# Optimization experiments

Hardware: AMD Instinct MI355X
Metric: run time of the kernel (lower is better)

## Reference

```python
import jax, jax.numpy as jnp
import numpy as np
from jax import lax

H = 64   # hidden_size
IN = 18  # input_size
L = 4    # lstm_layers
OUT = 3  # output_size
B = 2048
T = 512


def _lstm_layer(x, W_ih, W_hh, b_ih, b_hh):
    # x: [B,T,D]; PyTorch gate order: i, f, g, o
    xg = jnp.einsum('btd,gd->btg', x, W_ih) + b_ih + b_hh  # [B,T,4H]

    def step(carry, xg_t):
        h, c = carry
        gates = xg_t + h @ W_hh.T
        i, f, g, o = jnp.split(gates, 4, axis=-1)
        c = jax.nn.sigmoid(f) * c + jax.nn.sigmoid(i) * jnp.tanh(g)
        h = jax.nn.sigmoid(o) * jnp.tanh(c)
        return (h, c), h

    h0 = jnp.zeros((x.shape[0], H), x.dtype)
    _, hs = lax.scan(step, (h0, h0), jnp.swapaxes(xg, 0, 1))  # hs: [T,B,H]
    return jnp.swapaxes(hs, 0, 1)  # [B,T,H]


def _forward(x, Wi0, Wh0, bi0, bh0, Wi1, Wh1, bi1, bh1,
             Wi2, Wh2, bi2, bh2, Wi3, Wh3, bi3, bh3, W1, b1, W2, b2):
    h = x
    layers = [(Wi0, Wh0, bi0, bh0), (Wi1, Wh1, bi1, bh1),
              (Wi2, Wh2, bi2, bh2), (Wi3, Wh3, bi3, bh3)]
    for Wi, Wh, bi, bh in layers:
        h = _lstm_layer(h, Wi, Wh, bi, bh)
    last = h[:, -1, :]                      # [B,H]
    hid = jax.nn.relu(last @ W1.T + b1)     # [B,128]
    return hid @ W2.T + b2                  # [B,OUT]


def setup_inputs():
    key = jax.random.key(0)
    ks = jax.random.split(key, 1 + 4 * L + 4)
    d = {'x': jax.random.normal(ks[0], (B, T, IN), jnp.float32)}
    k = 1
    s = 0.1
    for l in range(L):
        din = IN if l == 0 else H
        d[f'Wi{l}'] = jax.random.normal(ks[k], (4 * H, din), jnp.float32) * s; k += 1
        d[f'Wh{l}'] = jax.random.normal(ks[k], (4 * H, H), jnp.float32) * s; k += 1
        d[f'bi{l}'] = jax.random.normal(ks[k], (4 * H,), jnp.float32) * s; k += 1
        d[f'bh{l}'] = jax.random.normal(ks[k], (4 * H,), jnp.float32) * s; k += 1
    d['W1'] = jax.random.normal(ks[k], (128, H), jnp.float32) * s; k += 1
    d['b1'] = jax.random.normal(ks[k], (128,), jnp.float32) * s; k += 1
    d['W2'] = jax.random.normal(ks[k], (OUT, 128), jnp.float32) * s; k += 1
    d['b2'] = jax.random.normal(ks[k], (OUT,), jnp.float32) * s
    return d


def reference(x, Wi0, Wh0, bi0, bh0, Wi1, Wh1, bi1, bh1,
              Wi2, Wh2, bi2, bh2, Wi3, Wh3, bi3, bh3, W1, b1, W2, b2):
    return _forward(x, Wi0, Wh0, bi0, bh0, Wi1, Wh1, bi1, bh1,
                    Wi2, Wh2, bi2, bh2, Wi3, Wh3, bi3, bh3, W1, b1, W2, b2)
```

## Files before the change

### kernel.cpp

```cpp
#include <hip/hip_runtime.h>
#include <stdint.h>

typedef __bf16 bf16_t;
typedef __bf16 bf16x8 __attribute__((ext_vector_type(8)));
typedef float  f32x4  __attribute__((ext_vector_type(4)));

union Frag { uint32_t u[4]; bf16x8 v; };

struct WPtrs {
    const float* Wi[4];
    const float* Wh[4];
    const float* bi[4];
    const float* bh[4];
};

#define LOG2E 1.44269504088896340736f

__device__ __forceinline__ float cell_c(float gi, float gf, float gg, float c) {
    const float ef = __builtin_amdgcn_exp2f(-gf);
    const float ei = __builtin_amdgcn_exp2f(-gi);
    const float Eg = __builtin_amdgcn_exp2f(gg);
    const float pf = 1.0f + ef, pi = 1.0f + ei;
    const float pg = Eg + 1.0f, mg = Eg - 1.0f;
    const float num = c * pi * pg + mg * pf;
    const float den = pf * pi * pg;
    return num * __builtin_amdgcn_rcpf(den);
}
__device__ __forceinline__ float cell_h(float go, float c) {
    const float Ec = __builtin_amdgcn_exp2f(c * (2.0f * LOG2E));
    const float eo = __builtin_amdgcn_exp2f(-go);
    const float num = Ec - 1.0f;
    const float den = (1.0f + eo) * (Ec + 1.0f);
    return num * __builtin_amdgcn_rcpf(den);
}

__device__ __forceinline__ float dpp_halfswap(float x) {
    int i = __float_as_int(x);
    int r = __builtin_amdgcn_update_dpp(i, i, 0x128 , 0xF, 0xF, false);
    return __int_as_float(r);
}

__global__ __launch_bounds__(1024, 4)
void lstm_fused(const float* __restrict__ x0, float* __restrict__ last_out, WPtrs wp)
{
    const int tile = blockIdx.x;
    const int tid  = threadIdx.x;
    const int w    = tid >> 6;
    const int lane = tid & 63;
    const int l15  = lane & 15;
    const int l4   = lane >> 4;
    const int l    = w >> 2;
    const int uq   = w & 3;
    const bool hiH = (l15 >= 8);
    const int  col = l15 & 7;

    __shared__ uint2 lds_h[2][4][64][6];

    for (int i = tid; i < 2 * 4 * 64 * 6; i += 1024)
        ((uint2*)lds_h)[i] = make_uint2(0u, 0u);

    const float* Wi = wp.Wi[l];
    const float* Wh = wp.Wh[l];

    const float gs[4] = {LOG2E, LOG2E, 2.0f * LOG2E, LOG2E};

    bf16x8 whA[4][2];
    bf16x8 wiA[4][2];
#pragma unroll
    for (int G = 0; G < 4; ++G) {
        const float sc = gs[G];
        const int row = G * 64 + 16 * uq + l15;
        const float* r = Wh + (size_t)row * 64;
#pragma unroll
        for (int s = 0; s < 2; ++s) {
            f32x4 a = *(const f32x4*)(r + 32 * s + 4 * l4);
            f32x4 b = *(const f32x4*)(r + 32 * s + 4 * l4 + 16);
            bf16x8 f;
            f[0] = (bf16_t)(a[0] * sc); f[1] = (bf16_t)(a[1] * sc);
            f[2] = (bf16_t)(a[2] * sc); f[3] = (bf16_t)(a[3] * sc);
            f[4] = (bf16_t)(b[0] * sc); f[5] = (bf16_t)(b[1] * sc);
            f[6] = (bf16_t)(b[2] * sc); f[7] = (bf16_t)(b[3] * sc);
            whA[G][s] = f;
        }
        if (l == 0) {
            const float* ri = Wi + (size_t)row * 18;
            const int k0 = 4 * l4;
            bf16x8 f;
            f[0] = (bf16_t)(ri[k0 + 0] * sc); f[1] = (bf16_t)(ri[k0 + 1] * sc);
            f[2] = (bf16_t)(ri[k0 + 2] * sc); f[3] = (bf16_t)(ri[k0 + 3] * sc);
            f[4] = (l4 == 0) ? (bf16_t)(ri[16] * sc) : (bf16_t)0.0f;
            f[5] = (l4 == 0) ? (bf16_t)(ri[17] * sc) : (bf16_t)0.0f;
            f[6] = (bf16_t)0.0f; f[7] = (bf16_t)0.0f;
            wiA[G][0] = f;
            wiA[G][1] = f;
        } else {
            const float* ri = Wi + (size_t)row * 64;
#pragma unroll
            for (int s = 0; s < 2; ++s) {
                f32x4 a = *(const f32x4*)(ri + 32 * s + 4 * l4);
                f32x4 b = *(const f32x4*)(ri + 32 * s + 4 * l4 + 16);
                bf16x8 f;
                f[0] = (bf16_t)(a[0] * sc); f[1] = (bf16_t)(a[1] * sc);
                f[2] = (bf16_t)(a[2] * sc); f[3] = (bf16_t)(a[3] * sc);
                f[4] = (bf16_t)(b[0] * sc); f[5] = (bf16_t)(b[1] * sc);
                f[6] = (bf16_t)(b[2] * sc); f[7] = (bf16_t)(b[3] * sc);
                wiA[G][s] = f;
            }
        }
    }

    float biasA[4], biasB[4];
#pragma unroll
    for (int G = 0; G < 4; ++G) {
        const int rb = G * 64 + 16 * uq + 4 * l4 + (hiH ? 2 : 0);
        biasA[G] = (wp.bi[l][rb]     + wp.bh[l][rb])     * gs[G];
        biasB[G] = (wp.bi[l][rb + 1] + wp.bh[l][rb + 1]) * gs[G];
    }

    bf16x8& xfA = wiA[2][1];
    bf16x8& xfB = wiA[3][1];
    const int    xbatch = tile * 8 + (hiH ? 7 : col);
    const float* xrow   = x0 + (size_t)xbatch * (512 * 18);
    auto loadx = [&](int t, bf16x8& dst) {
        const float* xr = xrow + t * 18;
        const int k0 = 4 * l4;
        bf16x8 f;
        f[0] = (bf16_t)xr[k0 + 0]; f[1] = (bf16_t)xr[k0 + 1];
        f[2] = (bf16_t)xr[k0 + 2]; f[3] = (bf16_t)xr[k0 + 3];
        f[4] = (l4 == 0) ? (bf16_t)xr[16] : (bf16_t)0.0f;
        f[5] = (l4 == 0) ? (bf16_t)xr[17] : (bf16_t)0.0f;
        f[6] = (bf16_t)0.0f; f[7] = (bf16_t)0.0f;
        dst = f;
    };
    if (l == 0) { loadx(0, xfA); loadx(1, xfB); }

    float c0 = 0.0f, c1 = 0.0f;

    __syncthreads();

    auto phase = [&](int p, int br, int bw, bf16x8& xf) {
        const int t = p - l;
        if (t >= 0 && t < 512) {
            const f32x4 z4 = {0.0f, 0.0f, 0.0f, 0.0f};
            f32x4 acc[4];

            if (l == 0) {
#pragma unroll
                for (int G = 0; G < 4; ++G)
                    acc[G] = __builtin_amdgcn_mfma_f32_16x16x32_bf16(wiA[G][0], xf, z4, 0, 0, 0);
                loadx((t + 2) & 511, xf);
            } else {
                Frag b0, b1;
                {
                    uint4 q0 = *(const uint4*)&lds_h[br][l - 1][lane][0];
                    uint4 q1 = *(const uint4*)&lds_h[br][l - 1][lane][2];
                    b0.u[0] = q0.x; b0.u[1] = q0.y; b0.u[2] = q0.z; b0.u[3] = q0.w;
                    b1.u[0] = q1.x; b1.u[1] = q1.y; b1.u[2] = q1.z; b1.u[3] = q1.w;
                }
#pragma unroll
                for (int G = 0; G < 4; ++G)
                    acc[G] = __builtin_amdgcn_mfma_f32_16x16x32_bf16(wiA[G][0], b0.v, z4, 0, 0, 0);
#pragma unroll
                for (int G = 0; G < 4; ++G)
                    acc[G] = __builtin_amdgcn_mfma_f32_16x16x32_bf16(wiA[G][1], b1.v, acc[G], 0, 0, 0);
            }

            {
                Frag h0, h1;
                uint4 q0 = *(const uint4*)&lds_h[br][l][lane][0];
                uint4 q1 = *(const uint4*)&lds_h[br][l][lane][2];
                h0.u[0] = q0.x; h0.u[1] = q0.y; h0.u[2] = q0.z; h0.u[3] = q0.w;
                h1.u[0] = q1.x; h1.u[1] = q1.y; h1.u[2] = q1.z; h1.u[3] = q1.w;
#pragma unroll
                for (int G = 0; G < 4; ++G)
                    acc[G] = __builtin_amdgcn_mfma_f32_16x16x32_bf16(whA[G][0], h0.v, acc[G], 0, 0, 0);
#pragma unroll
                for (int G = 0; G < 4; ++G)
                    acc[G] = __builtin_amdgcn_mfma_f32_16x16x32_bf16(whA[G][1], h1.v, acc[G], 0, 0, 0);
            }

            float g0[4], g1[4];
#pragma unroll
            for (int G = 0; G < 4; ++G) {
                const float s2 = dpp_halfswap(acc[G][2]);
                const float s3 = dpp_halfswap(acc[G][3]);
                g0[G] = (hiH ? s2 : acc[G][0]) + biasA[G];
                g1[G] = (hiH ? s3 : acc[G][1]) + biasB[G];
            }

            const float cA = cell_c(g0[0], g0[1], g0[2], c0);
            const float cB = cell_c(g1[0], g1[1], g1[2], c1);
            c0 = cA; c1 = cB;
            const float hA = cell_h(g0[3], cA);
            const float hB = cell_h(g1[3], cB);

            union { uint32_t u; bf16_t b[2]; } pk;
            pk.b[0] = (bf16_t)hA; pk.b[1] = (bf16_t)hB;
            uint32_t* slot = (uint32_t*)&lds_h[bw][l][16 * l4 + col][uq];
            slot[hiH ? 1 : 0] = pk.u;

            if (l == 3 && t == 511) {
                float* o = last_out + ((size_t)(tile * 8 + col)) * 64
                           + 16 * uq + 4 * l4 + (hiH ? 2 : 0);
                *(float2*)o = make_float2(hA, hB);
            }
        }
        __syncthreads();
    };

    for (int p = 0; p < 516; p += 2) {
        phase(p,     1, 0, xfA);
        phase(p + 1, 0, 1, xfB);
    }
}

__global__ __launch_bounds__(256)
void mlp_head(const float* __restrict__ last,
              const float* __restrict__ W1, const float* __restrict__ b1,
              const float* __restrict__ W2, const float* __restrict__ b2,
              float* __restrict__ out)
{
    __shared__ float sW1[128 * 64];
    __shared__ float sb1[128];
    __shared__ float sW2[3 * 128];
    __shared__ float sb2[4];
    const int tid = threadIdx.x;
    for (int i = tid; i < 128 * 64; i += 256) sW1[i] = W1[i];
    for (int i = tid; i < 128; i += 256) sb1[i] = b1[i];
    for (int i = tid; i < 3 * 128; i += 256) sW2[i] = W2[i];
    if (tid < 3) sb2[tid] = b2[tid];
    __syncthreads();

    const int b = blockIdx.x * 256 + tid;
    const float* lb = last + (size_t)b * 64;
    float xv[64];
#pragma unroll
    for (int k = 0; k < 64; k += 4) {
        f32x4 v = *(const f32x4*)(lb + k);
        xv[k] = v[0]; xv[k + 1] = v[1]; xv[k + 2] = v[2]; xv[k + 3] = v[3];
    }
    float o0 = sb2[0], o1 = sb2[1], o2 = sb2[2];
    for (int j = 0; j < 128; ++j) {
        float a = sb1[j];
        const float* wr = &sW1[j * 64];
#pragma unroll
        for (int k = 0; k < 64; k += 4) {
            f32x4 wv = *(const f32x4*)(wr + k);
            a += xv[k] * wv[0] + xv[k + 1] * wv[1] + xv[k + 2] * wv[2] + xv[k + 3] * wv[3];
        }
        a = fmaxf(a, 0.0f);
        o0 += a * sW2[0 * 128 + j];
        o1 += a * sW2[1 * 128 + j];
        o2 += a * sW2[2 * 128 + j];
    }
    out[(size_t)b * 3 + 0] = o0;
    out[(size_t)b * 3 + 1] = o1;
    out[(size_t)b * 3 + 2] = o2;
}

extern "C" void kernel_launch(void* const* d_in, const int* in_sizes, int n_in,
                              void* d_out, int out_size, void* d_ws, size_t ws_size,
                              hipStream_t stream)
{
    (void)in_sizes; (void)n_in; (void)out_size; (void)ws_size;

    const float* x = (const float*)d_in[0];
    WPtrs wp;
    for (int l = 0; l < 4; ++l) {
        wp.Wi[l] = (const float*)d_in[1 + 4 * l + 0];
        wp.Wh[l] = (const float*)d_in[1 + 4 * l + 1];
        wp.bi[l] = (const float*)d_in[1 + 4 * l + 2];
        wp.bh[l] = (const float*)d_in[1 + 4 * l + 3];
    }
    const float* W1 = (const float*)d_in[17];
    const float* b1 = (const float*)d_in[18];
    const float* W2 = (const float*)d_in[19];
    const float* b2 = (const float*)d_in[20];

    float* last = (float*)d_ws;

    lstm_fused<<<dim3(256), dim3(1024), 0, stream>>>(x, last, wp);
    mlp_head<<<dim3(8), dim3(256), 0, stream>>>(last, W1, b1, W2, b2, (float*)d_out);
}
```

Measured before the change: 581.4 us.

## Replace block-wide barriers with per-layer LDS counters and triple-buffered hidden state

Drops the __syncthreads between wavefront phases. Each layer's four waves now spin on shared-memory done counters that track their own layer, the layer above and the layer below, so layers can drift relative to each other instead of moving in lockstep. The hidden-state buffer grows from two slots to three so a layer can run ahead without overwriting data its neighbours still need. MFMA sections get raised wave priority and odd layers start with a staggered sleep, at the cost of spin-wait polling and atomics on every step.

```diff
diff --git a/kernel.cpp b/kernel.cpp
--- a/kernel.cpp
+++ b/kernel.cpp
@@ -54,14 +54,14 @@
     const bool hiH = (l15 >= 8);
     const int  col = l15 & 7;
 
-    __shared__ uint2 lds_h[2][4][64][6];
-
-    for (int i = tid; i < 2 * 4 * 64 * 6; i += 1024)
+    __shared__ uint2 lds_h[3][4][64][6];
+    __shared__ int   done4[4];
+    for (int i = tid; i < 3 * 4 * 64 * 6; i += 1024)
         ((uint2*)lds_h)[i] = make_uint2(0u, 0u);
+    if (tid < 4) done4[tid] = 0;
 
     const float* Wi = wp.Wi[l];
     const float* Wh = wp.Wh[l];
-
     const float gs[4] = {LOG2E, LOG2E, 2.0f * LOG2E, LOG2E};
 
     bf16x8 whA[4][2];
@@ -119,8 +119,7 @@
 
     bf16x8& xfA = wiA[2][1];
     bf16x8& xfB = wiA[3][1];
-    const int    xbatch = tile * 8 + (hiH ? 7 : col);
-    const float* xrow   = x0 + (size_t)xbatch * (512 * 18);
+    const float* xrow = x0 + (size_t)(tile * 8 + (hiH ? 7 : col)) * (512 * 18);
     auto loadx = [&](int t, bf16x8& dst) {
         const float* xr = xrow + t * 18;
         const int k0 = 4 * l4;
@@ -138,80 +137,100 @@
 
     __syncthreads();
 
-    auto phase = [&](int p, int br, int bw, bf16x8& xf) {
-        const int t = p - l;
-        if (t >= 0 && t < 512) {
-            const f32x4 z4 = {0.0f, 0.0f, 0.0f, 0.0f};
-            f32x4 acc[4];
-
-            if (l == 0) {
-#pragma unroll
-                for (int G = 0; G < 4; ++G)
-                    acc[G] = __builtin_amdgcn_mfma_f32_16x16x32_bf16(wiA[G][0], xf, z4, 0, 0, 0);
-                loadx((t + 2) & 511, xf);
-            } else {
-                Frag b0, b1;
-                {
-                    uint4 q0 = *(const uint4*)&lds_h[br][l - 1][lane][0];
-                    uint4 q1 = *(const uint4*)&lds_h[br][l - 1][lane][2];
-                    b0.u[0] = q0.x; b0.u[1] = q0.y; b0.u[2] = q0.z; b0.u[3] = q0.w;
-                    b1.u[0] = q1.x; b1.u[1] = q1.y; b1.u[2] = q1.z; b1.u[3] = q1.w;
-                }
-#pragma unroll
-                for (int G = 0; G < 4; ++G)
-                    acc[G] = __builtin_amdgcn_mfma_f32_16x16x32_bf16(wiA[G][0], b0.v, z4, 0, 0, 0);
-#pragma unroll
-                for (int G = 0; G < 4; ++G)
-                    acc[G] = __builtin_amdgcn_mfma_f32_16x16x32_bf16(wiA[G][1], b1.v, acc[G], 0, 0, 0);
+    volatile int* dp = done4;
+
+    auto step = [&](int t, int br, int bw, bf16x8& xf) {
+        {
+            const int needA = 4 * t, needU = 4 * (t + 1), needD = 4 * (t - 2);
+            for (;;) {
+                bool ok = (dp[l] >= needA);
+                if (l > 0) ok = ok && (dp[l - 1] >= needU);
+                if (l < 3) ok = ok && (dp[l + 1] >= needD);
+                if (ok) break;
+                __builtin_amdgcn_s_sleep(1);
             }
-
-            {
-                Frag h0, h1;
-                uint4 q0 = *(const uint4*)&lds_h[br][l][lane][0];
-                uint4 q1 = *(const uint4*)&lds_h[br][l][lane][2];
-                h0.u[0] = q0.x; h0.u[1] = q0.y; h0.u[2] = q0.z; h0.u[3] = q0.w;
-                h1.u[0] = q1.x; h1.u[1] = q1.y; h1.u[2] = q1.z; h1.u[3] = q1.w;
-#pragma unroll
-                for (int G = 0; G < 4; ++G)
-                    acc[G] = __builtin_amdgcn_mfma_f32_16x16x32_bf16(whA[G][0], h0.v, acc[G], 0, 0, 0);
-#pragma unroll
-                for (int G = 0; G < 4; ++G)
-                    acc[G] = __builtin_amdgcn_mfma_f32_16x16x32_bf16(whA[G][1], h1.v, acc[G], 0, 0, 0);
-            }
-
-            float g0[4], g1[4];
-#pragma unroll
-            for (int G = 0; G < 4; ++G) {
-                const float s2 = dpp_halfswap(acc[G][2]);
-                const float s3 = dpp_halfswap(acc[G][3]);
-                g0[G] = (hiH ? s2 : acc[G][0]) + biasA[G];
-                g1[G] = (hiH ? s3 : acc[G][1]) + biasB[G];
-            }
-
-            const float cA = cell_c(g0[0], g0[1], g0[2], c0);
-            const float cB = cell_c(g1[0], g1[1], g1[2], c1);
-            c0 = cA; c1 = cB;
-            const float hA = cell_h(g0[3], cA);
-            const float hB = cell_h(g1[3], cB);
-
-            union { uint32_t u; bf16_t b[2]; } pk;
-            pk.b[0] = (bf16_t)hA; pk.b[1] = (bf16_t)hB;
-            uint32_t* slot = (uint32_t*)&lds_h[bw][l][16 * l4 + col][uq];
-            slot[hiH ? 1 : 0] = pk.u;
-
-            if (l == 3 && t == 511) {
-                float* o = last_out + ((size_t)(tile * 8 + col)) * 64
-                           + 16 * uq + 4 * l4 + (hiH ? 2 : 0);
-                *(float2*)o = make_float2(hA, hB);
-            }
-        }
-        __syncthreads();
+            asm volatile("" ::: "memory");
+        }
+
+        const f32x4 z4 = {0.0f, 0.0f, 0.0f, 0.0f};
+        f32x4 acc[4];
+
+        __builtin_amdgcn_s_setprio(1);
+        if (l == 0) {
+#pragma unroll
+            for (int G = 0; G < 4; ++G)
+                acc[G] = __builtin_amdgcn_mfma_f32_16x16x32_bf16(wiA[G][0], xf, z4, 0, 0, 0);
+            loadx((t + 2) & 511, xf);
+        } else {
+            Frag b0, b1;
+            uint4 q0 = *(const uint4*)&lds_h[bw][l - 1][lane][0];
+            uint4 q1 = *(const uint4*)&lds_h[bw][l - 1][lane][2];
+            b0.u[0] = q0.x; b0.u[1] = q0.y; b0.u[2] = q0.z; b0.u[3] = q0.w;
+            b1.u[0] = q1.x; b1.u[1] = q1.y; b1.u[2] = q1.z; b1.u[3] = q1.w;
+#pragma unroll
+            for (int G = 0; G < 4; ++G)
+                acc[G] = __builtin_amdgcn_mfma_f32_16x16x32_bf16(wiA[G][0], b0.v, z4, 0, 0, 0);
+#pragma unroll
+            for (int G = 0; G < 4; ++G)
+                acc[G] = __builtin_amdgcn_mfma_f32_16x16x32_bf16(wiA[G][1], b1.v, acc[G], 0, 0, 0);
+        }
+        {
+            Frag h0, h1;
+            uint4 q0 = *(const uint4*)&lds_h[br][l][lane][0];
+            uint4 q1 = *(const uint4*)&lds_h[br][l][lane][2];
+            h0.u[0] = q0.x; h0.u[1] = q0.y; h0.u[2] = q0.z; h0.u[3] = q0.w;
+            h1.u[0] = q1.x; h1.u[1] = q1.y; h1.u[2] = q1.z; h1.u[3] = q1.w;
+#pragma unroll
+            for (int G = 0; G < 4; ++G)
+                acc[G] = __builtin_amdgcn_mfma_f32_16x16x32_bf16(whA[G][0], h0.v, acc[G], 0, 0, 0);
+#pragma unroll
+            for (int G = 0; G < 4; ++G)
+                acc[G] = __builtin_amdgcn_mfma_f32_16x16x32_bf16(whA[G][1], h1.v, acc[G], 0, 0, 0);
+        }
+        __builtin_amdgcn_s_setprio(0);
+
+        float g0[4], g1[4];
+#pragma unroll
+        for (int G = 0; G < 4; ++G) {
+            const float s2 = dpp_halfswap(acc[G][2]);
+            const float s3 = dpp_halfswap(acc[G][3]);
+            g0[G] = (hiH ? s2 : acc[G][0]) + biasA[G];
+            g1[G] = (hiH ? s3 : acc[G][1]) + biasB[G];
+        }
+        const float cA = cell_c(g0[0], g0[1], g0[2], c0);
+        const float cB = cell_c(g1[0], g1[1], g1[2], c1);
+        c0 = cA; c1 = cB;
+        const float hA = cell_h(g0[3], cA);
+        const float hB = cell_h(g1[3], cB);
+
+        union { uint32_t u; bf16_t b[2]; } pk;
+        pk.b[0] = (bf16_t)hA; pk.b[1] = (bf16_t)hB;
+        uint32_t* slot = (uint32_t*)&lds_h[bw][l][16 * l4 + col][uq];
+        slot[hiH ? 1 : 0] = pk.u;
+
+        if (l == 3 && t == 511) {
+            float* o = last_out + ((size_t)(tile * 8 + col)) * 64
+                       + 16 * uq + 4 * l4 + (hiH ? 2 : 0);
+            *(float2*)o = make_float2(hA, hB);
+        }
+
+        asm volatile("s_waitcnt lgkmcnt(0)" ::: "memory");
+        if (lane == 0) atomicAdd(&done4[l], 1);
+        asm volatile("" ::: "memory");
     };
 
-    for (int p = 0; p < 516; p += 2) {
-        phase(p,     1, 0, xfA);
-        phase(p + 1, 0, 1, xfB);
-    }
+    if (l & 1) { __builtin_amdgcn_s_sleep(8); __builtin_amdgcn_s_sleep(8); }
+
+    for (int t = 0; t < 510; t += 6) {
+        step(t + 0, 2, 0, xfA);
+        step(t + 1, 0, 1, xfB);
+        step(t + 2, 1, 2, xfA);
+        step(t + 3, 2, 0, xfB);
+        step(t + 4, 0, 1, xfA);
+        step(t + 5, 1, 2, xfB);
+    }
+    step(510, 2, 0, xfA);
+    step(511, 0, 1, xfB);
 }
 
 __global__ __launch_bounds__(256)
```

After: 622.8 us. 1.07x slower.
